# Optimization experiments

Hardware: AMD Instinct MI355X
Metric: run time of the kernel (lower is better)

## Reference

```python
import jax, jax.numpy as jnp
import numpy as np

N_NODES = 100000
H_FEATS = 128
N_TRIPLETS = 500000


def setup_inputs() -> dict:
    key = jax.random.key(0)
    k_h, k_t, k_w1, k_b1, k_w2, k_b2 = jax.random.split(key, 6)
    h = jax.random.normal(k_h, (N_NODES, H_FEATS), dtype=jnp.float32)
    triplets = jax.random.randint(k_t, (N_TRIPLETS, 3), 0, N_NODES, dtype=jnp.int64)
    # nn.Linear weights: [out, in]
    W1_w = jax.random.normal(k_w1, (H_FEATS, 3 * H_FEATS), dtype=jnp.float32) * 0.05
    W1_b = jax.random.normal(k_b1, (H_FEATS,), dtype=jnp.float32) * 0.05
    W2_w = jax.random.normal(k_w2, (2, H_FEATS), dtype=jnp.float32) * 0.05
    W2_b = jax.random.normal(k_b2, (2,), dtype=jnp.float32) * 0.05
    return {"h": h, "triplets": triplets, "W1_w": W1_w, "W1_b": W1_b,
            "W2_w": W2_w, "W2_b": W2_b}


def reference(h, triplets, W1_w, W1_b, W2_w, W2_b):
    # gather: [T, 3, H] -> [T, 3*H]
    T = triplets.shape[0]
    emb = h[triplets].reshape(T, 3 * H_FEATS)
    hid = jax.nn.relu(emb @ W1_w.T + W1_b)   # [T, H]
    out = hid @ W2_w.T + W2_b                # [T, 2]
    return out
```

## Files before the change

kernel.cpp:

```cpp
#include <hip/hip_runtime.h>

typedef __bf16 bf16x8 __attribute__((ext_vector_type(8)));
typedef float f32x4 __attribute__((ext_vector_type(4)));

__device__ __forceinline__ unsigned short f2bf(float x) {
  union { float f; unsigned int i; } u; u.f = x;
  return (unsigned short)((u.i + 0x7FFFu + ((u.i >> 16) & 1u)) >> 16);
}
__device__ __forceinline__ float bf2f(unsigned short b) {
  union { unsigned int i; float f; } u; u.i = ((unsigned int)b) << 16;
  return u.f;
}
__device__ __forceinline__ bf16x8 cvt8(float4 a, float4 b) {
  union { unsigned short u[8]; bf16x8 v; } r;
  r.u[0] = f2bf(a.x); r.u[1] = f2bf(a.y); r.u[2] = f2bf(a.z); r.u[3] = f2bf(a.w);
  r.u[4] = f2bf(b.x); r.u[5] = f2bf(b.y); r.u[6] = f2bf(b.z); r.u[7] = f2bf(b.w);
  return r.v;
}

__global__ void pack_w1_kernel(const float* __restrict__ W1w, uint4* __restrict__ wp) {
  int fid = blockIdx.x * 256 + threadIdx.x;
  int kk = fid / 1536;
  int rem = fid - kk * 1536;
  int nf = rem >> 6;
  int ln = rem & 63;
  int ng = nf * 16 + (ln & 15);
  int c = ng & 127;
  int jp = ng >> 7;
  int k0 = kk * 32 + (ln >> 4) * 8;
  const float* src = W1w + (size_t)c * 384 + jp * 128 + k0;
  float4 a = *(const float4*)src;
  float4 b = *(const float4*)(src + 4);
  union { unsigned short u[8]; uint4 v; } r;
  r.u[0] = f2bf(a.x); r.u[1] = f2bf(a.y); r.u[2] = f2bf(a.z); r.u[3] = f2bf(a.w);
  r.u[4] = f2bf(b.x); r.u[5] = f2bf(b.y); r.u[6] = f2bf(b.z); r.u[7] = f2bf(b.w);
  wp[fid] = r.v;
}

__global__ __launch_bounds__(512, 6) void phaseA_kernel(
    const float* __restrict__ h, const uint4* __restrict__ wp,
    unsigned short* __restrict__ P, int Nn) {
  __shared__ uint4 wl[48 * 64];
  const int tid = threadIdx.x;
  const int cs = blockIdx.x & 1;
  const int tile = blockIdx.x >> 1;

  for (int i = tid; i < 48 * 64; i += 512) {
    int fr = i >> 6;
    int ln = i & 63;
    int kk = fr / 12, nfl = fr - kk * 12;
    wl[i] = wp[(kk * 24 + cs * 12 + nfl) * 64 + ln];
  }
  __syncthreads();

  const int lane = tid & 63;
  const int wv = tid >> 6;
  const int rg = wv >> 1;
  const int cg = wv & 1;
  const int l15 = lane & 15;
  const int lg = lane >> 4;

  const int mb = tile * 64 + rg * 16;
  int arow = mb + l15;
  if (arow >= Nn) arow = Nn - 1;
  const float* ap = h + (size_t)arow * 128 + lg * 8;

  f32x4 acc[6];
#pragma unroll
  for (int nf = 0; nf < 6; nf++) acc[nf] = (f32x4){0.f, 0.f, 0.f, 0.f};

#pragma unroll
  for (int kk = 0; kk < 4; kk++) {
    bf16x8 af = cvt8(*(const float4*)(ap + kk * 32), *(const float4*)(ap + kk * 32 + 4));
#pragma unroll
    for (int nf = 0; nf < 6; nf++) {
      bf16x8 bf = __builtin_bit_cast(bf16x8, wl[(kk * 12 + cg * 6 + nf) * 64 + lane]);
      acc[nf] = __builtin_amdgcn_mfma_f32_16x16x32_bf16(af, bf, acc[nf], 0, 0, 0);
    }
  }
#pragma unroll
  for (int nf = 0; nf < 6; nf++) {
#pragma unroll
    for (int r = 0; r < 4; r++) {
      int row = mb + lg * 4 + r;
      if (row < Nn)
        P[(size_t)row * 384 + cs * 192 + cg * 96 + nf * 16 + l15] = f2bf(acc[nf][r]);
    }
  }
}

__global__ __launch_bounds__(256) void phaseB_kernel(
    const unsigned short* __restrict__ P, const int* __restrict__ trip,
    const float* __restrict__ b1, const float* __restrict__ W2w,
    const float* __restrict__ b2, float* __restrict__ out, int T) {
  constexpr int U = 5;
  const int gtid = blockIdx.x * 256 + threadIdx.x;
  const int g0 = gtid >> 4;
  const int c8 = threadIdx.x & 15;
  const int ng = (gridDim.x * 256) >> 4;
  const int c0 = c8 * 8;

  float4 b1a = *(const float4*)(b1 + c0), b1b = *(const float4*)(b1 + c0 + 4);
  float4 w0a = *(const float4*)(W2w + c0), w0b = *(const float4*)(W2w + c0 + 4);
  float4 w1a = *(const float4*)(W2w + 128 + c0), w1b = *(const float4*)(W2w + 128 + c0 + 4);
  const float bb0 = b2[0], bb1 = b2[1];
  float b1r[8] = {b1a.x, b1a.y, b1a.z, b1a.w, b1b.x, b1b.y, b1b.z, b1b.w};
  float w20[8] = {w0a.x, w0a.y, w0a.z, w0a.w, w0b.x, w0b.y, w0b.z, w0b.w};
  float w21[8] = {w1a.x, w1a.y, w1a.z, w1a.w, w1b.x, w1b.y, w1b.z, w1b.w};

  for (int t = g0; t < T; t += U * ng) {
    int tc[U];
    bool hv[U];
#pragma unroll
    for (int u = 0; u < U; u++) {
      int tt = t + u * ng;
      hv[u] = tt < T;
      tc[u] = hv[u] ? tt : t;
    }
    union { uint4 v; unsigned short u[8]; } va[U][3];
#pragma unroll
    for (int u = 0; u < U; u++) {
      int i0 = trip[3 * tc[u]], i1 = trip[3 * tc[u] + 1], i2 = trip[3 * tc[u] + 2];
      va[u][0].v = *((const uint4*)(P + (size_t)i0 * 384) + c8);
      va[u][1].v = *((const uint4*)(P + (size_t)i1 * 384 + 128) + c8);
      va[u][2].v = *((const uint4*)(P + (size_t)i2 * 384 + 256) + c8);
    }
    float p0[U], p1[U];
#pragma unroll
    for (int u = 0; u < U; u++) {
      p0[u] = 0.f; p1[u] = 0.f;
#pragma unroll
      for (int j = 0; j < 8; j++) {
        float s = bf2f(va[u][0].u[j]) + bf2f(va[u][1].u[j]) + bf2f(va[u][2].u[j]) + b1r[j];
        s = fmaxf(s, 0.f);
        p0[u] = fmaf(s, w20[j], p0[u]);
        p1[u] = fmaf(s, w21[j], p1[u]);
      }
    }
#pragma unroll
    for (int d = 1; d < 16; d <<= 1) {
#pragma unroll
      for (int u = 0; u < U; u++) {
        p0[u] += __shfl_xor(p0[u], d);
        p1[u] += __shfl_xor(p1[u], d);
      }
    }
    if (c8 == 0) {
#pragma unroll
      for (int u = 0; u < U; u++) {
        if (hv[u]) {
          float2 o;
          o.x = p0[u] + bb0;
          o.y = p1[u] + bb1;
          *(float2*)(out + (size_t)(t + u * ng) * 2) = o;
        }
      }
    }
  }
}

__global__ __launch_bounds__(512, 2) void fused_fallback(
    const float* __restrict__ Hsrc, const int* __restrict__ trip,
    const float* __restrict__ W1w, const float* __restrict__ b1,
    const float* __restrict__ W2w, const float* __restrict__ b2,
    float* __restrict__ out, int T) {
  extern __shared__ unsigned short w1p[];
  const int tid = threadIdx.x;
  for (int f = tid; f < 6144; f += 512) {
    int kk = f >> 9; int nf = (f >> 6) & 7; int ln = f & 63;
    int row = nf * 16 + (ln & 15); int k0 = kk * 32 + (ln >> 4) * 8;
    const float* src = W1w + row * 384 + k0;
    float4 a = *(const float4*)src; float4 b = *(const float4*)(src + 4);
    union { unsigned short u[8]; uint4 v; } r;
    r.u[0] = f2bf(a.x); r.u[1] = f2bf(a.y); r.u[2] = f2bf(a.z); r.u[3] = f2bf(a.w);
    r.u[4] = f2bf(b.x); r.u[5] = f2bf(b.y); r.u[6] = f2bf(b.z); r.u[7] = f2bf(b.w);
    *(uint4*)&w1p[f * 8] = r.v;
  }
  __syncthreads();
  const int lane = tid & 63, wv = tid >> 6, l15 = lane & 15, lg = lane >> 4;
  float b1r[8], w20[8], w21[8];
#pragma unroll
  for (int nf = 0; nf < 8; nf++) {
    int c = nf * 16 + l15;
    b1r[nf] = b1[c]; w20[nf] = W2w[c]; w21[nf] = W2w[128 + c];
  }
  const float bb0 = b2[0], bb1 = b2[1];
  const int ntiles = (T + 511) >> 9;
  for (int tile = blockIdx.x; tile < ntiles; tile += gridDim.x) {
    const int base = tile * 512 + wv * 64;
    f32x4 acc[4][8];
#pragma unroll
    for (int m = 0; m < 4; m++)
#pragma unroll
      for (int nf = 0; nf < 8; nf++) acc[m][nf] = (f32x4){0.f, 0.f, 0.f, 0.f};
    int off[4][3];
#pragma unroll
    for (int m = 0; m < 4; m++) {
      int row = base + m * 16 + l15;
      int rc = row < T ? row : T - 1;
      off[m][0] = trip[rc * 3]; off[m][1] = trip[rc * 3 + 1]; off[m][2] = trip[rc * 3 + 2];
    }
#pragma unroll
    for (int part = 0; part < 3; part++)
#pragma unroll
      for (int kq = 0; kq < 4; kq++) {
        const int kk = part * 4 + kq;
        bf16x8 af[4];
#pragma unroll
        for (int m = 0; m < 4; m++) {
          const float* p = Hsrc + ((size_t)off[m][part] << 7) + kq * 32 + lg * 8;
          af[m] = cvt8(*(const float4*)p, *(const float4*)(p + 4));
        }
#pragma unroll
        for (int nf = 0; nf < 8; nf++) {
          bf16x8 bf = __builtin_bit_cast(bf16x8,
              *(const uint4*)&w1p[(size_t)(kk * 512 + nf * 64 + lane) * 8]);
#pragma unroll
          for (int m = 0; m < 4; m++)
            acc[m][nf] = __builtin_amdgcn_mfma_f32_16x16x32_bf16(af[m], bf, acc[m][nf], 0, 0, 0);
        }
      }
#pragma unroll
    for (int m = 0; m < 4; m++) {
      float p0[4] = {0, 0, 0, 0}, p1[4] = {0, 0, 0, 0};
#pragma unroll
      for (int nf = 0; nf < 8; nf++)
#pragma unroll
        for (int r = 0; r < 4; r++) {
          float hv = fmaxf(acc[m][nf][r] + b1r[nf], 0.f);
          p0[r] = fmaf(hv, w20[nf], p0[r]);
          p1[r] = fmaf(hv, w21[nf], p1[r]);
        }
#pragma unroll
      for (int d = 1; d < 16; d <<= 1)
#pragma unroll
        for (int r = 0; r < 4; r++) {
          p0[r] += __shfl_xor(p0[r], d);
          p1[r] += __shfl_xor(p1[r], d);
        }
#pragma unroll
      for (int r = 0; r < 4; r++)
        if (l15 == r) {
          int row = base + m * 16 + lg * 4 + r;
          if (row < T) {
            float2 o; o.x = p0[r] + bb0; o.y = p1[r] + bb1;
            *(float2*)(out + (size_t)row * 2) = o;
          }
        }
    }
  }
}

extern "C" void kernel_launch(void* const* d_in, const int* in_sizes, int n_in,
                              void* d_out, int out_size, void* d_ws, size_t ws_size,
                              hipStream_t stream) {
  const float* h = (const float*)d_in[0];
  const int* trip = (const int*)d_in[1];
  const float* W1w = (const float*)d_in[2];
  const float* b1 = (const float*)d_in[3];
  const float* W2w = (const float*)d_in[4];
  const float* b2 = (const float*)d_in[5];
  float* out = (float*)d_out;

  const int Nn = in_sizes[0] / 128;
  const int T = in_sizes[1] / 3;
  const size_t pbytes = (size_t)Nn * 384 * 2;
  const size_t need = pbytes + 6144 * 16;

  if (ws_size >= need) {
    unsigned short* P = (unsigned short*)d_ws;
    uint4* wp = (uint4*)((char*)d_ws + pbytes);
    pack_w1_kernel<<<24, 256, 0, stream>>>(W1w, wp);
    const int ntiles = (Nn + 63) >> 6;
    phaseA_kernel<<<ntiles * 2, 512, 0, stream>>>(h, wp, P, Nn);
    phaseB_kernel<<<2048, 256, 0, stream>>>(P, trip, b1, W2w, b2, out, T);
  } else {
    fused_fallback<<<256, 512, 6144 * 16, stream>>>(h, trip, W1w, b1, W2w, b2, out, T);
  }
}
```

Baseline: 105.2 us.

## Stage phaseA outputs through LDS for coalesced stores and remap blocks across XCDs

Phase A now writes its bf16 MFMA accumulators into shared memory, reusing the weight buffer with a padded stride, and then stores them to P as contiguous 16-byte vectors. Before, each thread issued scattered 2-byte global stores. Block indices are also remapped so the two column halves of a tile land on the same XCD, which should improve L2 locality for the shared h rows. The cost is an extra LDS round trip, two barriers, and some idle blocks created by padding the grid to a multiple of 8.

```diff
diff --git a/kernel.cpp b/kernel.cpp
--- a/kernel.cpp
+++ b/kernel.cpp
@@ -37,13 +37,18 @@
   wp[fid] = r.v;
 }
 
+#define OT_STRIDE 200
 __global__ __launch_bounds__(512, 6) void phaseA_kernel(
     const float* __restrict__ h, const uint4* __restrict__ wp,
-    unsigned short* __restrict__ P, int Nn) {
+    unsigned short* __restrict__ P, int Nn, int ntiles) {
   __shared__ uint4 wl[48 * 64];
   const int tid = threadIdx.x;
-  const int cs = blockIdx.x & 1;
-  const int tile = blockIdx.x >> 1;
+  const int b = blockIdx.x;
+  const int xcd = b & 7;
+  const int j = b >> 3;
+  const int cs = j & 1;
+  const int tile = (j >> 1) * 8 + xcd;
+  if (tile >= ntiles) return;
 
   for (int i = tid; i < 48 * 64; i += 512) {
     int fr = i >> 6;
@@ -78,13 +83,33 @@
       acc[nf] = __builtin_amdgcn_mfma_f32_16x16x32_bf16(af, bf, acc[nf], 0, 0, 0);
     }
   }
-#pragma unroll
-  for (int nf = 0; nf < 6; nf++) {
-#pragma unroll
-    for (int r = 0; r < 4; r++) {
-      int row = mb + lg * 4 + r;
-      if (row < Nn)
-        P[(size_t)row * 384 + cs * 192 + cg * 96 + nf * 16 + l15] = f2bf(acc[nf][r]);
+
+  __syncthreads();
+  unsigned short* ot = (unsigned short*)wl;
+#pragma unroll
+  for (int nf = 0; nf < 6; nf++)
+#pragma unroll
+    for (int r = 0; r < 4; r++)
+      ot[(rg * 16 + lg * 4 + r) * OT_STRIDE + cg * 96 + nf * 16 + l15] =
+          f2bf(acc[nf][r]);
+  __syncthreads();
+
+  const int r0 = tile * 64;
+  if (r0 + 64 <= Nn) {
+#pragma unroll
+    for (int pass = 0; pass < 3; pass++) {
+      int i = pass * 512 + tid;
+      int row = i / 24, c = i - row * 24;
+      uint4 v = *(const uint4*)&ot[row * OT_STRIDE + c * 8];
+      *(uint4*)(P + (size_t)(r0 + row) * 384 + cs * 192 + c * 8) = v;
+    }
+  } else {
+    for (int i = tid; i < 64 * 24; i += 512) {
+      int row = i / 24, c = i - row * 24;
+      if (r0 + row < Nn) {
+        uint4 v = *(const uint4*)&ot[row * OT_STRIDE + c * 8];
+        *(uint4*)(P + (size_t)(r0 + row) * 384 + cs * 192 + c * 8) = v;
+      }
     }
   }
 }
@@ -272,7 +297,8 @@
     uint4* wp = (uint4*)((char*)d_ws + pbytes);
     pack_w1_kernel<<<24, 256, 0, stream>>>(W1w, wp);
     const int ntiles = (Nn + 63) >> 6;
-    phaseA_kernel<<<ntiles * 2, 512, 0, stream>>>(h, wp, P, Nn);
+    const int ntp = ((ntiles + 7) >> 3) << 3;
+    phaseA_kernel<<<ntp * 2, 512, 0, stream>>>(h, wp, P, Nn, ntiles);
     phaseB_kernel<<<2048, 256, 0, stream>>>(P, trip, b1, W2w, b2, out, T);
   } else {
     fused_fallback<<<256, 512, 6144 * 16, stream>>>(h, trip, W1w, b1, W2w, b2, out, T);
```

Result: faster. 102.3 us (median of 2 runs) (-2.8%).
